# Performance work log

Measured on AMD Instinct MI355X. Metric: run time of the kernel, lower is better.

Reference implementation:

```python
import jax, jax.numpy as jnp
import numpy as np

D_MODEL, N_HEADS, LATENT, ROPE = 4096, 128, 512, 64
HEAD_DIM = D_MODEL // N_HEADS  # 32
B, S = 2, 1024


def setup_inputs() -> dict:
    key = jax.random.key(0)
    ks = jax.random.split(key, 9)
    def w(k, i, o):
        return jax.random.normal(k, (i, o), dtype=jnp.float32) * (1.0 / np.sqrt(i))
    return {
        "x": jax.random.normal(ks[0], (B, S, D_MODEL), dtype=jnp.float32),
        "Wq_down": w(ks[1], D_MODEL, LATENT),
        "Wq_up": w(ks[2], LATENT, N_HEADS * HEAD_DIM),
        "Wq_rope": w(ks[3], D_MODEL, N_HEADS * ROPE),
        "Wkv_down": w(ks[4], D_MODEL, LATENT),
        "Wk_up": w(ks[5], LATENT, N_HEADS * HEAD_DIM),
        "Wv_up": w(ks[6], LATENT, N_HEADS * HEAD_DIM),
        "Wk_rope": w(ks[7], D_MODEL, ROPE),
        "Wo": w(ks[8], N_HEADS * HEAD_DIM, D_MODEL),
    }


def reference(x, Wq_down, Wq_up, Wq_rope, Wkv_down, Wk_up, Wv_up, Wk_rope, Wo):
    b, s, _ = x.shape
    # latent down-projections
    c_q = x @ Wq_down                                   # [B,S,latent]
    c_kv = x @ Wkv_down                                 # [B,S,latent]
    # up-projections, reshaped to per-head
    q_c = (c_q @ Wq_up).reshape(b, s, N_HEADS, HEAD_DIM)    # [B,S,H,Dh]
    q_r = (x @ Wq_rope).reshape(b, s, N_HEADS, ROPE)        # [B,S,H,Dr]
    k_c = (c_kv @ Wk_up).reshape(b, s, N_HEADS, HEAD_DIM)   # [B,S,H,Dh]
    v_c = (c_kv @ Wv_up).reshape(b, s, N_HEADS, HEAD_DIM)   # [B,S,H,Dh]
    k_r = x @ Wk_rope                                       # [B,S,Dr] shared over heads
    scale = jnp.asarray((HEAD_DIM + ROPE) ** 0.5, x.dtype)
    # scores = q.k with q=[q_c|q_r], k=[k_c|k_r(broadcast)] -> split the dot product
    scores = (jnp.einsum("bqhd,bkhd->bhqk", q_c, k_c)
              + jnp.einsum("bqhd,bkd->bhqk", q_r, k_r)) / scale  # [B,H,S,S]
    attn = jax.nn.softmax(scores, axis=-1)
    out = jnp.einsum("bhqk,bkhd->bqhd", attn, v_c)          # [B,S,H,Dh]
    out = out.reshape(b, s, N_HEADS * HEAD_DIM)
    return out @ Wo                                         # [B,S,d_model]
```

## Files before the change

kernel.cpp:

```cpp
#include <hip/hip_runtime.h>
#include <hip/hip_bf16.h>
#include <math.h>

#define D_MODEL 4096
#define N_HEADS 128
#define LATENT  512
#define ROPE_D  64
#define HEAD_D  32
#define BATCH   2
#define SEQ     1024
#define NTOK    (BATCH*SEQ)

typedef unsigned short u16;
typedef __attribute__((ext_vector_type(8))) short bf16x8;
typedef __attribute__((ext_vector_type(4))) float f32x4;

__device__ __forceinline__ u16 f2bf(float f) {
    union { float f; unsigned u; } v; v.f = f;
    unsigned r = (v.u + 0x7fffu + ((v.u >> 16) & 1u)) >> 16;
    return (u16)r;
}

__device__ __forceinline__ void gl_lds16(const u16* g, u16* l) {
    __builtin_amdgcn_global_load_lds(
        (const __attribute__((address_space(1))) unsigned int*)g,
        (__attribute__((address_space(3))) unsigned int*)l, 16, 0, 0);
}

__global__ __launch_bounds__(256)
void cast_x_kernel(const float* __restrict__ in, u16* __restrict__ out)
{
    size_t i = ((size_t)blockIdx.x * 256 + threadIdx.x) * 8;
    float4 a = *(const float4*)(in + i);
    float4 b = *(const float4*)(in + i + 4);
    u16 o[8] = {f2bf(a.x), f2bf(a.y), f2bf(a.z), f2bf(a.w),
                f2bf(b.x), f2bf(b.y), f2bf(b.z), f2bf(b.w)};
    *(bf16x8*)(out + i) = *(bf16x8*)o;
}

__global__ __launch_bounds__(256)
void castT_kernel(const float* __restrict__ W, u16* __restrict__ Wt,
                  int K, int N)
{
    __shared__ float tile[32][33];
    const int tid = threadIdx.x;
    const int j0 = blockIdx.x * 32;
    const int i0 = blockIdx.y * 32;
    #pragma unroll
    for (int it = 0; it < 4; ++it) {
        int e = tid + it * 256;
        int r = e >> 5, c = e & 31;
        tile[r][c] = (j0 + c < N) ? W[(size_t)(i0 + r) * N + j0 + c] : 0.f;
    }
    __syncthreads();
    #pragma unroll
    for (int it = 0; it < 4; ++it) {
        int e = tid + it * 256;
        int n = e >> 5, k = e & 31;
        Wt[(size_t)(j0 + n) * K + i0 + k] = f2bf(tile[k][n]);
    }
}

template<int OUTF32>
__global__ __launch_bounds__(512)
void gemm8p(const u16* __restrict__ A, const u16* __restrict__ Bt,
            void* __restrict__ Cout, int M, int N, int K,
            int lda, int ldb, int ldc)
{
    constexpr int TILE_A = 256 * 64;
    constexpr int TILE_B = 128 * 64;
    constexpr int SLOT   = TILE_A + TILE_B;

    extern __shared__ __align__(16) u16 lds[];

    const int tid  = threadIdx.x;
    const int lane = tid & 63;
    const int wave = tid >> 6;
    const int wr = wave >> 2, wc = wave & 3;
    const int l15 = lane & 15, lg = lane >> 4;

    const int nwg  = gridDim.x * gridDim.y;
    const int orig = blockIdx.y * gridDim.x + blockIdx.x;
    const int swz  = (orig & 7) * (nwg >> 3) + (orig >> 3);
    const int bm = (swz / gridDim.x) * 256, bn = (swz % gridDim.x) * 128;

    const int NT = K >> 6;

    auto stageA = [&](int t) {
        u16* base = lds + (t % 3) * SLOT;
        const int kt = t << 6;
        #pragma unroll
        for (int it = 0; it < 4; ++it) {
            int f = it * 512 + tid;
            int row = f >> 3, c = f & 7;
            int sc = c ^ (row & 7);
            gl_lds16(A + (size_t)(bm + row) * lda + kt + sc * 8, base + f * 8);
        }
    };
    auto stageB = [&](int t) {
        u16* base = lds + (t % 3) * SLOT + TILE_A;
        const int kt = t << 6;
        #pragma unroll
        for (int it = 0; it < 2; ++it) {
            int f = it * 512 + tid;
            int row = f >> 3, c = f & 7;
            int sc = c ^ (row & 7);
            gl_lds16(Bt + (size_t)(bn + row) * ldb + kt + sc * 8, base + f * 8);
        }
    };

    f32x4 acc[8][2];
    #pragma unroll
    for (int m = 0; m < 8; ++m) {
        acc[m][0] = (f32x4){0.f, 0.f, 0.f, 0.f};
        acc[m][1] = (f32x4){0.f, 0.f, 0.f, 0.f};
    }

    stageA(0); stageB(0); stageA(1); stageB(1);
    asm volatile("s_waitcnt vmcnt(6)" ::: "memory");
    __builtin_amdgcn_sched_barrier(0);
    __builtin_amdgcn_s_barrier();
    __builtin_amdgcn_sched_barrier(0);

    for (int t = 0; t < NT; ++t) {
        const u16* bA = lds + (t % 3) * SLOT;
        const u16* bB = bA + TILE_A;
        #pragma unroll
        for (int s = 0; s < 2; ++s) {
            bf16x8 af[8], bfr[2];
            #pragma unroll
            for (int m = 0; m < 8; ++m) {
                int row = wr * 128 + m * 16 + l15;
                int ch = (s * 4 + lg) ^ (row & 7);
                af[m] = *(const bf16x8*)(bA + row * 64 + ch * 8);
            }
            #pragma unroll
            for (int n = 0; n < 2; ++n) {
                int row = wc * 32 + n * 16 + l15;
                int ch = (s * 4 + lg) ^ (row & 7);
                bfr[n] = *(const bf16x8*)(bB + row * 64 + ch * 8);
            }
            if (s == 0) {
                if (t + 2 < NT) stageA(t + 2);
            } else {
                if (t + 2 < NT) stageB(t + 2);
                if (t + 1 < NT) {
                    if (t + 2 < NT) asm volatile("s_waitcnt vmcnt(6)" ::: "memory");
                    else            asm volatile("s_waitcnt vmcnt(0)" ::: "memory");
                }
            }
            asm volatile("" ::: "memory");
            __builtin_amdgcn_sched_barrier(0);
            __builtin_amdgcn_s_barrier();
            __builtin_amdgcn_sched_barrier(0);
            __builtin_amdgcn_s_setprio(1);
            #pragma unroll
            for (int m = 0; m < 8; ++m) {
                acc[m][0] = __builtin_amdgcn_mfma_f32_16x16x32_bf16(af[m], bfr[0], acc[m][0], 0, 0, 0);
                acc[m][1] = __builtin_amdgcn_mfma_f32_16x16x32_bf16(af[m], bfr[1], acc[m][1], 0, 0, 0);
            }
            __builtin_amdgcn_s_setprio(0);
            __builtin_amdgcn_sched_barrier(0);
            __builtin_amdgcn_s_barrier();
            __builtin_amdgcn_sched_barrier(0);
            asm volatile("" ::: "memory");
        }
    }

    #pragma unroll
    for (int m = 0; m < 8; ++m)
        #pragma unroll
        for (int n = 0; n < 2; ++n)
            #pragma unroll
            for (int ri = 0; ri < 4; ++ri) {
                int row = bm + wr * 128 + m * 16 + 4 * lg + ri;
                int col = bn + wc * 32 + n * 16 + l15;
                float v = acc[m][n][ri];
                if (OUTF32) ((float*)Cout)[(size_t)row * ldc + col] = v;
                else        ((u16*)Cout)[(size_t)row * ldc + col] = f2bf(v);
            }
}

__global__ __launch_bounds__(256)
void vtrans_kernel(const u16* __restrict__ vc, u16* __restrict__ vt)
{
    __shared__ __align__(16) u16 tile[64][72];
    const int tid = threadIdx.x;
    const int c0 = blockIdx.x * 64;
    const int s0 = blockIdx.y * 64;
    const int b  = blockIdx.z;
    #pragma unroll
    for (int it = 0; it < 2; ++it) {
        int e = it * 256 + tid;
        int r = e >> 3, c8 = e & 7;
        *(bf16x8*)&tile[r][c8 * 8] =
            *(const bf16x8*)(vc + (size_t)(b * SEQ + s0 + r) * 8192 + c0 + c8 * 8);
    }
    __syncthreads();
    #pragma unroll
    for (int it = 0; it < 2; ++it) {
        int e = it * 256 + tid;
        int d = e >> 3, c8 = e & 7;
        u16 o[8];
        #pragma unroll
        for (int j = 0; j < 8; ++j) o[j] = tile[c8 * 8 + j][d];
        *(bf16x8*)(vt + (size_t)(b * D_MODEL + c0 + d) * SEQ + s0 + c8 * 8) = *(bf16x8*)o;
    }
}

__global__ __launch_bounds__(256)
void attn_kernel(const u16* __restrict__ q_c, const u16* __restrict__ q_r,
                 const u16* __restrict__ k_c, const u16* __restrict__ k_r,
                 const u16* __restrict__ vt,  u16* __restrict__ attn_out)
{
    __shared__ __align__(16) u16 s_kc[2][64 * 32];
    __shared__ __align__(16) u16 s_kr[2][64 * 64];
    __shared__ __align__(16) u16 s_vt[2][32 * 64];
    __shared__ __align__(16) u16 s_p[4][16 * 64];

    const int tid  = threadIdx.x;
    const int lane = tid & 63;
    const int w    = tid >> 6;
    const int l15  = lane & 15, lg = lane >> 4;
    const int q0 = blockIdx.x * 64;
    const int h  = blockIdx.y;
    const int b  = blockIdx.z;
    const size_t bS = (size_t)b * SEQ;
    const int hc = h * HEAD_D;
    const float c2 = 0.1020620726159658f * 1.44269504088896f;

    const int qrow = q0 + w * 16 + l15;
    const bf16x8 qf0 = *(const bf16x8*)(q_c + (bS + qrow) * 4096 + hc + lg * 8);
    const bf16x8 qf1 = *(const bf16x8*)(q_r + (bS + qrow) * 9344 + h * ROPE_D + lg * 8);
    const bf16x8 qf2 = *(const bf16x8*)(q_r + (bS + qrow) * 9344 + h * ROPE_D + 32 + lg * 8);

    float m2 = -1e30f, lsum = 0.f;
    f32x4 oacc[2];
    oacc[0] = (f32x4){0.f, 0.f, 0.f, 0.f};
    oacc[1] = (f32x4){0.f, 0.f, 0.f, 0.f};

    auto stage = [&](int buf, int k0) {
        { int f = tid, r = f >> 2, c = f & 3;
          gl_lds16(k_c + (bS + k0 + r) * 8192 + hc + ((c ^ (r & 3)) << 3),
                   &s_kc[buf][f * 8]); }
        #pragma unroll
        for (int it = 0; it < 2; ++it) {
          int f = it * 256 + tid, r = f >> 3, c = f & 7;
          gl_lds16(k_r + (bS + k0 + r) * 9344 + ((c ^ (r & 7)) << 3),
                   &s_kr[buf][f * 8]); }
        { int f = tid, d = f >> 3, c = f & 7;
          gl_lds16(vt + ((size_t)b * D_MODEL + hc + d) * SEQ + k0 + ((c ^ (d & 7)) << 3),
                   &s_vt[buf][f * 8]); }
    };

    stage(0, 0);
    __syncthreads();

    int cur = 0;
    for (int t = 0; t < SEQ / 64; ++t) {
        if (t + 1 < SEQ / 64) stage(cur ^ 1, (t + 1) * 64);

        f32x4 sc[4];
        #pragma unroll
        for (int fc = 0; fc < 4; ++fc) sc[fc] = (f32x4){0.f, 0.f, 0.f, 0.f};
        __builtin_amdgcn_s_setprio(1);
        #pragma unroll
        for (int fc = 0; fc < 4; ++fc) {
            int row = fc * 16 + l15;
            bf16x8 kb = *(const bf16x8*)&s_kc[cur][row * 32 + ((lg ^ (row & 3)) << 3)];
            sc[fc] = __builtin_amdgcn_mfma_f32_16x16x32_bf16(kb, qf0, sc[fc], 0, 0, 0);
        }
        #pragma unroll
        for (int tt = 0; tt < 2; ++tt) {
            bf16x8 qf = tt ? qf2 : qf1;
            #pragma unroll
            for (int fc = 0; fc < 4; ++fc) {
                int row = fc * 16 + l15;
                bf16x8 kb = *(const bf16x8*)&s_kr[cur][row * 64 + (((tt * 4 + lg) ^ (row & 7)) << 3)];
                sc[fc] = __builtin_amdgcn_mfma_f32_16x16x32_bf16(kb, qf, sc[fc], 0, 0, 0);
            }
        }
        __builtin_amdgcn_s_setprio(0);

        float tmx = sc[0][0];
        #pragma unroll
        for (int fc = 0; fc < 4; ++fc)
            #pragma unroll
            for (int ri = 0; ri < 4; ++ri)
                tmx = fmaxf(tmx, sc[fc][ri]);
        tmx = fmaxf(tmx, __shfl_xor(tmx, 16));
        tmx = fmaxf(tmx, __shfl_xor(tmx, 32));
        float tl2 = tmx * c2;
        if (!__all(tl2 <= m2 + 8.f)) {
            float mn = fmaxf(m2, tl2);
            float corr = exp2f(m2 - mn);
            m2 = mn;
            lsum *= corr;
            #pragma unroll
            for (int ri = 0; ri < 4; ++ri) {
                float cr = __shfl(corr, 4 * lg + ri);
                oacc[0][ri] *= cr; oacc[1][ri] *= cr;
            }
        }
        float rs = 0.f;
        unsigned pk0[4], pk1[4];
        #pragma unroll
        for (int fc = 0; fc < 4; ++fc) {
            float p0 = exp2f(fmaf(sc[fc][0], c2, -m2));
            float p1 = exp2f(fmaf(sc[fc][1], c2, -m2));
            float p2 = exp2f(fmaf(sc[fc][2], c2, -m2));
            float p3 = exp2f(fmaf(sc[fc][3], c2, -m2));
            rs += (p0 + p1) + (p2 + p3);
            asm("v_cvt_pk_bf16_f32 %0, %1, %2" : "=v"(pk0[fc]) : "v"(p0), "v"(p1));
            asm("v_cvt_pk_bf16_f32 %0, %1, %2" : "=v"(pk1[fc]) : "v"(p2), "v"(p3));
        }
        rs += __shfl_xor(rs, 16);
        rs += __shfl_xor(rs, 32);
        lsum += rs;
        #pragma unroll
        for (int fc = 0; fc < 4; ++fc) {
            int ch = (2 * fc + (lg >> 1)) ^ (l15 & 7);
            *(uint2*)&s_p[w][l15 * 64 + ch * 8 + 4 * (lg & 1)] =
                make_uint2(pk0[fc], pk1[fc]);
        }

        __builtin_amdgcn_s_setprio(1);
        #pragma unroll
        for (int t2 = 0; t2 < 2; ++t2) {
            bf16x8 pa = *(const bf16x8*)&s_p[w][l15 * 64 + (((t2 * 4 + lg) ^ (l15 & 7)) << 3)];
            #pragma unroll
            for (int fd = 0; fd < 2; ++fd) {
                int row = fd * 16 + l15;
                bf16x8 vb = *(const bf16x8*)&s_vt[cur][row * 64 + (((t2 * 4 + lg) ^ (row & 7)) << 3)];
                oacc[fd] = __builtin_amdgcn_mfma_f32_16x16x32_bf16(pa, vb, oacc[fd], 0, 0, 0);
            }
        }
        __builtin_amdgcn_s_setprio(0);

        __syncthreads();
        cur ^= 1;
    }

    #pragma unroll
    for (int ri = 0; ri < 4; ++ri) {
        float ls = __shfl(lsum, 4 * lg + ri);
        float inv = 1.f / ls;
        int row = q0 + w * 16 + 4 * lg + ri;
        attn_out[(bS + row) * 4096 + hc + l15]      = f2bf(oacc[0][ri] * inv);
        attn_out[(bS + row) * 4096 + hc + 16 + l15] = f2bf(oacc[1][ri] * inv);
    }
}

extern "C" void kernel_launch(void* const* d_in, const int* in_sizes, int n_in,
                              void* d_out, int out_size, void* d_ws, size_t ws_size,
                              hipStream_t stream)
{
    (void)in_sizes; (void)n_in; (void)out_size; (void)ws_size;

    const float* x        = (const float*)d_in[0];
    const float* Wq_down  = (const float*)d_in[1];
    const float* Wq_up    = (const float*)d_in[2];
    const float* Wq_rope  = (const float*)d_in[3];
    const float* Wkv_down = (const float*)d_in[4];
    const float* Wk_up    = (const float*)d_in[5];
    const float* Wv_up    = (const float*)d_in[6];
    const float* Wk_rope  = (const float*)d_in[7];
    const float* Wo       = (const float*)d_in[8];

    u16* ws   = (u16*)d_ws;
    u16* xb   = ws;
    u16* BigT = xb + (size_t)8388608;
    u16* UpT  = BigT + (size_t)38797312;
    u16* WuqT = UpT + (size_t)4194304;
    u16* C_big= WuqT + (size_t)2097152;
    u16* C2   = C_big + (size_t)19136512;
    u16* WoT  = BigT;
    u16* vt   = BigT + (size_t)16777216;
    u16* q_c  = BigT + (size_t)25165824;
    u16* attn_out = xb;

    dim3 blk(256);

    (void)hipFuncSetAttribute((const void*)&gemm8p<0>,
                              hipFuncAttributeMaxDynamicSharedMemorySize, 147456);
    (void)hipFuncSetAttribute((const void*)&gemm8p<1>,
                              hipFuncAttributeMaxDynamicSharedMemorySize, 147456);

    hipMemsetAsync(BigT + (size_t)9280 * 4096, 0, (size_t)64 * 4096 * 2, stream);
    hipLaunchKernelGGL(cast_x_kernel, dim3(4096), blk, 0, stream, x, xb);
    hipLaunchKernelGGL(castT_kernel, dim3(256, 128), blk, 0, stream, Wq_rope, BigT, 4096, 8192);
    hipLaunchKernelGGL(castT_kernel, dim3(16, 128), blk, 0, stream, Wq_down, BigT + (size_t)8192 * 4096, 4096, 512);
    hipLaunchKernelGGL(castT_kernel, dim3(16, 128), blk, 0, stream, Wkv_down, BigT + (size_t)8704 * 4096, 4096, 512);
    hipLaunchKernelGGL(castT_kernel, dim3(2, 128), blk, 0, stream, Wk_rope, BigT + (size_t)9216 * 4096, 4096, 64);
    hipLaunchKernelGGL(castT_kernel, dim3(128, 16), blk, 0, stream, Wk_up, UpT, 512, 4096);
    hipLaunchKernelGGL(castT_kernel, dim3(128, 16), blk, 0, stream, Wv_up, UpT + (size_t)4096 * 512, 512, 4096);
    hipLaunchKernelGGL(castT_kernel, dim3(128, 16), blk, 0, stream, Wq_up, WuqT, 512, 4096);

    gemm8p<0><<<dim3(73, 8), dim3(512), 147456, stream>>>(
        xb, BigT, C_big, NTOK, 9344, 4096, 4096, 4096, 9344);
    hipLaunchKernelGGL(castT_kernel, dim3(128, 128), blk, 0, stream, Wo, WoT, 4096, 4096);
    gemm8p<0><<<dim3(64, 8), dim3(512), 147456, stream>>>(
        C_big + 8704, UpT, C2, NTOK, 8192, 512, 9344, 512, 8192);
    gemm8p<0><<<dim3(32, 8), dim3(512), 147456, stream>>>(
        C_big + 8192, WuqT, q_c, NTOK, 4096, 512, 9344, 512, 4096);
    hipLaunchKernelGGL(vtrans_kernel, dim3(64, 16, 2), blk, 0, stream, C2 + 4096, vt);
    hipLaunchKernelGGL(attn_kernel, dim3(16, 128, 2), blk, 0, stream,
                       q_c, C_big, C2, C_big + 9216, vt, attn_out);
    gemm8p<1><<<dim3(32, 8), dim3(512), 147456, stream>>>(
        attn_out, WoT, d_out, NTOK, 4096, 4096, 4096, 4096, 4096);
}
```

Measured before the change: 584.3 us.

## Add 128x128 single-buffered GEMM, vectorize castT, relax attention barriers

Adds a simpler 256-thread 128x128-tile bf16 GEMM with static LDS and uses it for the large fused down-projection and the output projection instead of the triple-buffered 256x128 kernel. The tile remapping of gemm8p changes so the swizzled block walks M first. castT now loads float4 and stores four bf16 at once, and the attention loop replaces __syncthreads with explicit vmcnt/lgkmcnt waits so the next-tile prefetch can stay in flight. The new GEMM has no software pipelining, so load latency may become exposed in exchange for higher occupancy and more blocks.

```diff
diff --git a/kernel.cpp b/kernel.cpp
--- a/kernel.cpp
+++ b/kernel.cpp
@@ -46,19 +46,103 @@
     const int tid = threadIdx.x;
     const int j0 = blockIdx.x * 32;
     const int i0 = blockIdx.y * 32;
-    #pragma unroll
-    for (int it = 0; it < 4; ++it) {
-        int e = tid + it * 256;
-        int r = e >> 5, c = e & 31;
-        tile[r][c] = (j0 + c < N) ? W[(size_t)(i0 + r) * N + j0 + c] : 0.f;
+    {
+        int r = tid >> 3, c4 = (tid & 7) << 2;
+        float4 v = *(const float4*)(W + (size_t)(i0 + r) * N + j0 + c4);
+        tile[r][c4 + 0] = v.x; tile[r][c4 + 1] = v.y;
+        tile[r][c4 + 2] = v.z; tile[r][c4 + 3] = v.w;
     }
     __syncthreads();
-    #pragma unroll
-    for (int it = 0; it < 4; ++it) {
-        int e = tid + it * 256;
-        int n = e >> 5, k = e & 31;
-        Wt[(size_t)(j0 + n) * K + i0 + k] = f2bf(tile[k][n]);
-    }
+    {
+        int n = tid >> 3, k4 = (tid & 7) << 2;
+        u16 o[4] = { f2bf(tile[k4 + 0][n]), f2bf(tile[k4 + 1][n]),
+                     f2bf(tile[k4 + 2][n]), f2bf(tile[k4 + 3][n]) };
+        *(uint2*)(Wt + (size_t)(j0 + n) * K + i0 + k4) = *(uint2*)o;
+    }
+}
+
+template<int OUTF32>
+__global__ __launch_bounds__(256)
+void gemm_bf16(const u16* __restrict__ A, const u16* __restrict__ Bt,
+               void* __restrict__ Cout, int M, int N, int K,
+               int lda, int ldb, int ldc)
+{
+    __shared__ __align__(16) u16 As[128 * 64];
+    __shared__ __align__(16) u16 Bs[128 * 64];
+
+    const int tid  = threadIdx.x;
+    const int lane = tid & 63;
+    const int wave = tid >> 6;
+    const int wr = wave >> 1, wc = wave & 1;
+    const int nwg  = gridDim.x * gridDim.y;
+    const int orig = blockIdx.y * gridDim.x + blockIdx.x;
+    const int swz  = (orig & 7) * (nwg >> 3) + (orig >> 3);
+    const int bm = (swz % gridDim.y) * 128;
+    const int bn = (swz / gridDim.y) * 128;
+    const int l15 = lane & 15, lg = lane >> 4;
+
+    f32x4 acc[4][4];
+    #pragma unroll
+    for (int i = 0; i < 4; ++i)
+        #pragma unroll
+        for (int j = 0; j < 4; ++j) acc[i][j] = (f32x4){0.f, 0.f, 0.f, 0.f};
+
+    for (int kt = 0; kt < K; kt += 64) {
+        __syncthreads();
+        #pragma unroll
+        for (int i = 0; i < 4; ++i) {
+            int f = i * 256 + tid;
+            int row = f >> 3, c = f & 7;
+            int sc = c ^ (row & 7);
+            gl_lds16(A + (size_t)(bm + row) * lda + kt + sc * 8, As + f * 8);
+        }
+        #pragma unroll
+        for (int i = 0; i < 4; ++i) {
+            int f = i * 256 + tid;
+            int row = f >> 3, c = f & 7;
+            int sc = c ^ (row & 7);
+            gl_lds16(Bt + (size_t)(bn + row) * ldb + kt + sc * 8, Bs + f * 8);
+        }
+        __syncthreads();
+
+        #pragma unroll
+        for (int t = 0; t < 2; ++t) {
+            bf16x8 af[4], bf[4];
+            #pragma unroll
+            for (int fm = 0; fm < 4; ++fm) {
+                int row = wr * 64 + fm * 16 + l15;
+                int c = (t * 4 + lg) ^ (row & 7);
+                af[fm] = *(const bf16x8*)(As + row * 64 + c * 8);
+            }
+            #pragma unroll
+            for (int fn = 0; fn < 4; ++fn) {
+                int row = wc * 64 + fn * 16 + l15;
+                int c = (t * 4 + lg) ^ (row & 7);
+                bf[fn] = *(const bf16x8*)(Bs + row * 64 + c * 8);
+            }
+            #pragma unroll
+            for (int fm = 0; fm < 4; ++fm)
+                #pragma unroll
+                for (int fn = 0; fn < 4; ++fn)
+                    acc[fm][fn] = __builtin_amdgcn_mfma_f32_16x16x32_bf16(
+                        af[fm], bf[fn], acc[fm][fn], 0, 0, 0);
+        }
+    }
+
+    #pragma unroll
+    for (int fm = 0; fm < 4; ++fm)
+        #pragma unroll
+        for (int fn = 0; fn < 4; ++fn)
+            #pragma unroll
+            for (int ri = 0; ri < 4; ++ri) {
+                int row = bm + wr * 64 + fm * 16 + 4 * lg + ri;
+                int col = bn + wc * 64 + fn * 16 + l15;
+                if (col < N) {
+                    float v = acc[fm][fn][ri];
+                    if (OUTF32) ((float*)Cout)[(size_t)row * ldc + col] = v;
+                    else        ((u16*)Cout)[(size_t)row * ldc + col] = f2bf(v);
+                }
+            }
 }
 
 template<int OUTF32>
@@ -82,7 +166,8 @@
     const int nwg  = gridDim.x * gridDim.y;
     const int orig = blockIdx.y * gridDim.x + blockIdx.x;
     const int swz  = (orig & 7) * (nwg >> 3) + (orig >> 3);
-    const int bm = (swz / gridDim.x) * 256, bn = (swz % gridDim.x) * 128;
+    const int bm = (swz % gridDim.y) * 256;
+    const int bn = (swz / gridDim.y) * 128;
 
     const int NT = K >> 6;
 
@@ -254,11 +339,22 @@
     };
 
     stage(0, 0);
-    __syncthreads();
+    asm volatile("s_waitcnt vmcnt(0)" ::: "memory");
+    __builtin_amdgcn_sched_barrier(0);
+    __builtin_amdgcn_s_barrier();
+    __builtin_amdgcn_sched_barrier(0);
 
     int cur = 0;
     for (int t = 0; t < SEQ / 64; ++t) {
-        if (t + 1 < SEQ / 64) stage(cur ^ 1, (t + 1) * 64);
+        if (t + 1 < SEQ / 64) {
+            stage(cur ^ 1, (t + 1) * 64);
+            asm volatile("s_waitcnt vmcnt(4)" ::: "memory");
+        } else {
+            asm volatile("s_waitcnt vmcnt(0)" ::: "memory");
+        }
+        __builtin_amdgcn_sched_barrier(0);
+        __builtin_amdgcn_s_barrier();
+        __builtin_amdgcn_sched_barrier(0);
 
         f32x4 sc[4];
         #pragma unroll
@@ -337,7 +433,10 @@
         }
         __builtin_amdgcn_s_setprio(0);
 
-        __syncthreads();
+        asm volatile("s_waitcnt lgkmcnt(0)" ::: "memory");
+        __builtin_amdgcn_sched_barrier(0);
+        __builtin_amdgcn_s_barrier();
+        __builtin_amdgcn_sched_barrier(0);
         cur ^= 1;
     }
 
@@ -383,8 +482,6 @@
 
     (void)hipFuncSetAttribute((const void*)&gemm8p<0>,
                               hipFuncAttributeMaxDynamicSharedMemorySize, 147456);
-    (void)hipFuncSetAttribute((const void*)&gemm8p<1>,
-                              hipFuncAttributeMaxDynamicSharedMemorySize, 147456);
 
     hipMemsetAsync(BigT + (size_t)9280 * 4096, 0, (size_t)64 * 4096 * 2, stream);
     hipLaunchKernelGGL(cast_x_kernel, dim3(4096), blk, 0, stream, x, xb);
@@ -396,7 +493,7 @@
     hipLaunchKernelGGL(castT_kernel, dim3(128, 16), blk, 0, stream, Wv_up, UpT + (size_t)4096 * 512, 512, 4096);
     hipLaunchKernelGGL(castT_kernel, dim3(128, 16), blk, 0, stream, Wq_up, WuqT, 512, 4096);
 
-    gemm8p<0><<<dim3(73, 8), dim3(512), 147456, stream>>>(
+    gemm_bf16<0><<<dim3(73, 16), blk, 0, stream>>>(
         xb, BigT, C_big, NTOK, 9344, 4096, 4096, 4096, 9344);
     hipLaunchKernelGGL(castT_kernel, dim3(128, 128), blk, 0, stream, Wo, WoT, 4096, 4096);
     gemm8p<0><<<dim3(64, 8), dim3(512), 147456, stream>>>(
@@ -406,6 +503,6 @@
     hipLaunchKernelGGL(vtrans_kernel, dim3(64, 16, 2), blk, 0, stream, C2 + 4096, vt);
     hipLaunchKernelGGL(attn_kernel, dim3(16, 128, 2), blk, 0, stream,
                        q_c, C_big, C2, C_big + 9216, vt, attn_out);
-    gemm8p<1><<<dim3(32, 8), dim3(512), 147456, stream>>>(
+    gemm_bf16<1><<<dim3(32, 16), blk, 0, stream>>>(
         attn_out, WoT, d_out, NTOK, 4096, 4096, 4096, 4096, 4096);
 }
```

New measurement: 545.8 us. -6.6%, faster.
